# Kernel optimization log

Measured on AMD Instinct MI355X. Metric: run time of the kernel, lower is better.

## Reference

```python
import jax, jax.numpy as jnp
import numpy as np

EPS = 1e-4


def bin_act(x):
    # row-wise standardize (torch std is unbiased, ddof=1) then XNOR-style binarize
    mu = x.mean(axis=1, keepdims=True)
    sd = x.std(axis=1, ddof=1, keepdims=True)
    xn = (x - mu) / (sd + EPS)
    alpha = jnp.abs(xn).mean(axis=1, keepdims=True)  # L1 norm / n
    return alpha * jnp.sign(xn)


def bin_linear(inp, w, b):
    # BinLinearFunction.forward: w_hat = sign(w) * (||w_row||_1 / n_in)
    n = w.shape[1]
    m = jnp.abs(w).sum(axis=1, keepdims=True) / n
    w_hat = jnp.sign(w) * m
    return inp @ w_hat.T + b


def scatter_mean(feat, dst, n_dst):
    s = jax.ops.segment_sum(feat, dst, num_segments=n_dst)
    cnt = jax.ops.segment_sum(jnp.ones(dst.shape, feat.dtype), dst, num_segments=n_dst)
    return s / jnp.maximum(cnt, 1.0)[:, None]


def sage_layer(x, src, dst, n_dst, w_rel, b_rel, w_root, b_root):
    xb = bin_act(x)
    xt = bin_act(x[:n_dst])
    agg = scatter_mean(xb[src], dst, n_dst)  # mean aggregation of binarized neighbors
    return bin_linear(agg, w_rel, b_rel) + bin_linear(xt, w_root, b_root)


def setup_inputs() -> dict:
    key = jax.random.key(0)
    ks = jax.random.split(key, 10)
    N0, N1, N2 = 512000, 20480, 2048
    E1, E2 = 512000, 20480
    IN, HID, OUT = 128, 256, 64
    x = jax.random.normal(ks[0], (N0, IN), dtype=jnp.float32)
    src1 = jax.random.randint(ks[1], (E1,), 0, N0)
    dst1 = jax.random.randint(ks[2], (E1,), 0, N1)
    src2 = jax.random.randint(ks[3], (E2,), 0, N1)
    dst2 = jax.random.randint(ks[4], (E2,), 0, N2)
    def winit(k, out_f, in_f):
        return jax.random.normal(k, (out_f, in_f), dtype=jnp.float32) * np.sqrt(1.0 / in_f)
    return {
        "x": x, "src1": src1, "dst1": dst1, "src2": src2, "dst2": dst2,
        "w_rel1": winit(ks[5], HID, IN), "b_rel1": jnp.zeros((HID,), jnp.float32),
        "w_root1": winit(ks[6], HID, IN), "b_root1": jnp.zeros((HID,), jnp.float32),
        "w_rel2": winit(ks[7], OUT, HID), "b_rel2": jnp.zeros((OUT,), jnp.float32),
        "w_root2": winit(ks[8], OUT, HID), "b_root2": jnp.zeros((OUT,), jnp.float32),
        "n1": N1, "n2": N2,
    }


def reference(x, src1, dst1, src2, dst2, w_rel1, b_rel1, w_root1, b_root1,
              w_rel2, b_rel2, w_root2, b_root2, n1, n2):
    h = sage_layer(x, src1, dst1, n1, w_rel1, b_rel1, w_root1, b_root1)
    h = jax.nn.relu(h)  # dropout p=0.0
    h = sage_layer(h, src2, dst2, n2, w_rel2, b_rel2, w_root2, b_root2)
    return jax.nn.log_softmax(h, axis=-1)
```

## Files before the change

### kernel.cpp

```cpp
#include <hip/hip_runtime.h>
#include <stdint.h>

typedef unsigned long long u64;
typedef float nfloat4 __attribute__((ext_vector_type(4)));


#define CAP1 128
#define CAP2 128

__device__ __forceinline__ void pack_row128(
    float4 v0, float4 v1, float4 v2, float4 v3, float mu, int c,
    u64& w0, u64& w1)
{
  unsigned m = 0;
  m |= (v0.x > mu) ? 1u << 0  : 0u;
  m |= (v0.y > mu) ? 1u << 1  : 0u;
  m |= (v0.z > mu) ? 1u << 2  : 0u;
  m |= (v0.w > mu) ? 1u << 3  : 0u;
  m |= (v1.x > mu) ? 1u << 4  : 0u;
  m |= (v1.y > mu) ? 1u << 5  : 0u;
  m |= (v1.z > mu) ? 1u << 6  : 0u;
  m |= (v1.w > mu) ? 1u << 7  : 0u;
  m |= (v2.x > mu) ? 1u << 8  : 0u;
  m |= (v2.y > mu) ? 1u << 9  : 0u;
  m |= (v2.z > mu) ? 1u << 10 : 0u;
  m |= (v2.w > mu) ? 1u << 11 : 0u;
  m |= (v3.x > mu) ? 1u << 12 : 0u;
  m |= (v3.y > mu) ? 1u << 13 : 0u;
  m |= (v3.z > mu) ? 1u << 14 : 0u;
  m |= (v3.w > mu) ? 1u << 15 : 0u;
  u64 wv = (u64)m << (16 * (c & 3));
  wv |= __shfl_xor(wv, 1);
  wv |= __shfl_xor(wv, 2);
  u64 other = __shfl_xor(wv, 4);
  w0 = (c & 4) ? other : wv;
  w1 = (c & 4) ? wv : other;
}

__device__ __forceinline__ void prep_w128_block(
    const float* __restrict__ w, int rowbase, int tid,
    ulonglong2* __restrict__ wbits, float* __restrict__ m)
{
  int lane = tid & 63;
  int g = lane >> 3, c = lane & 7;
  int row = rowbase + (tid >> 6) * 8 + g;
  const float4* wr = (const float4*)(w + (size_t)row * 128);
  float4 v0 = wr[c];
  float4 v1 = wr[c + 8];
  float4 v2 = wr[c + 16];
  float4 v3 = wr[c + 24];
  float s = fabsf(v0.x) + fabsf(v0.y) + fabsf(v0.z) + fabsf(v0.w)
          + fabsf(v1.x) + fabsf(v1.y) + fabsf(v1.z) + fabsf(v1.w)
          + fabsf(v2.x) + fabsf(v2.y) + fabsf(v2.z) + fabsf(v2.w)
          + fabsf(v3.x) + fabsf(v3.y) + fabsf(v3.z) + fabsf(v3.w);
  s += __shfl_xor(s, 1); s += __shfl_xor(s, 2); s += __shfl_xor(s, 4);
  u64 w0, w1;
  pack_row128(v0, v1, v2, v3, 0.0f, c, w0, w1);
  if (c == 0) {
    wbits[row] = make_ulonglong2(w0, w1);
    m[row] = s * (1.0f / 128.0f);
  }
}

__device__ __forceinline__ void prep_w256_block(
    const float* __restrict__ w, int rowbase, int tid,
    u64* __restrict__ wbits, float* __restrict__ m)
{
  int lane = tid & 63;
  int o = rowbase + (tid >> 6);
  const float* wr = w + (size_t)o * 256;
  float s = 0.0f;
  u64 b[4];
  #pragma unroll
  for (int wd = 0; wd < 4; wd++) {
    float v = wr[wd * 64 + lane];
    s += fabsf(v);
    b[wd] = __ballot(v > 0.0f);
  }
  #pragma unroll
  for (int off = 32; off > 0; off >>= 1) s += __shfl_xor(s, off);
  if (lane == 0) {
    wbits[o * 4 + 0] = b[0]; wbits[o * 4 + 1] = b[1];
    wbits[o * 4 + 2] = b[2]; wbits[o * 4 + 3] = b[3];
    m[o] = s * (1.0f / 256.0f);
  }
}

__global__ __launch_bounds__(256) void prep_all_kernel(
    const float* __restrict__ w_rel1, const float* __restrict__ w_root1,
    const float* __restrict__ w_rel2, const float* __restrict__ w_root2,
    ulonglong2* __restrict__ wbr1, float* __restrict__ m_r1,
    ulonglong2* __restrict__ wbt1, float* __restrict__ m_t1,
    u64* __restrict__ wbr2, float* __restrict__ m_r2,
    u64* __restrict__ wbt2, float* __restrict__ m_t2,
    int* __restrict__ cnt, int cntn,
    int* __restrict__ markw, int markn)
{
  int b = blockIdx.x, t = threadIdx.x;
  if (b < 8) {
    prep_w128_block(w_rel1, b * 32, t, wbr1, m_r1);
  } else if (b < 16) {
    prep_w128_block(w_root1, (b - 8) * 32, t, wbt1, m_t1);
  } else if (b < 32) {
    prep_w256_block(w_rel2, (b - 16) * 4, t, wbr2, m_r2);
  } else if (b < 48) {
    prep_w256_block(w_root2, (b - 32) * 4, t, wbt2, m_t2);
  } else if (b < 59) {
    int base = (b - 48) * 2048 + t * 8;
    #pragma unroll
    for (int k = 0; k < 8; k++) {
      int i = base + k;
      if (i < cntn) cnt[i] = 0;
    }
  } else {
    int base = (b - 59) * 2048 + t * 8;
    #pragma unroll
    for (int k = 0; k < 8; k++) {
      int i = base + k;
      if (i < markn) markw[i] = 0;
    }
  }
}

__global__ void scatter_direct_kernel(
    const int* __restrict__ dst1, const int* __restrict__ src1, int E1,
    int* __restrict__ cnt1, int* __restrict__ slots1,
    const int* __restrict__ dst2, const int* __restrict__ src2, int E2,
    int* __restrict__ cnt2, int* __restrict__ slots2,
    unsigned char* __restrict__ mark)
{
  int i = blockIdx.x * blockDim.x + threadIdx.x;
  if (i < E1) {
    int s = src1[i];
    mark[s] = 1;
    int dd = dst1[i];
    int p = atomicAdd(&cnt1[dd], 1);
    if (p < CAP1) slots1[(size_t)dd * CAP1 + p] = s;
  } else if (i < E1 + E2) {
    int j = i - E1;
    int dd = dst2[j];
    int p = atomicAdd(&cnt2[dd], 1);
    if (p < CAP2) slots2[(size_t)dd * CAP2 + p] = src2[j];
  }
}

__global__ __launch_bounds__(256) void binact128_kernel(
    const float* __restrict__ x, const unsigned char* __restrict__ mark,
    int n1, u64* __restrict__ rec)
{
  int lane = threadIdx.x & 63;
  int wid  = blockIdx.x * 4 + (threadIdx.x >> 6);
  int g = lane >> 3;
  int c = lane & 7;
  int row = wid * 8 + g;
  if (row >= n1 && mark[row] == 0) return;

  const nfloat4* xr = (const nfloat4*)(x + (size_t)row * 128);
  nfloat4 n0 = __builtin_nontemporal_load(xr + c);
  nfloat4 n1v = __builtin_nontemporal_load(xr + c + 8);
  nfloat4 n2 = __builtin_nontemporal_load(xr + c + 16);
  nfloat4 n3 = __builtin_nontemporal_load(xr + c + 24);
  float4 v0 = make_float4(n0.x, n0.y, n0.z, n0.w);
  float4 v1 = make_float4(n1v.x, n1v.y, n1v.z, n1v.w);
  float4 v2 = make_float4(n2.x, n2.y, n2.z, n2.w);
  float4 v3 = make_float4(n3.x, n3.y, n3.z, n3.w);

  float s = (v0.x + v0.y + v0.z + v0.w) + (v1.x + v1.y + v1.z + v1.w)
          + (v2.x + v2.y + v2.z + v2.w) + (v3.x + v3.y + v3.z + v3.w);
  s += __shfl_xor(s, 1); s += __shfl_xor(s, 2); s += __shfl_xor(s, 4);
  float mu = s * (1.0f / 128.0f);

  float ss = 0.f, sa = 0.f;
  {
    float d;
    d = v0.x - mu; ss += d * d; sa += fabsf(d);
    d = v0.y - mu; ss += d * d; sa += fabsf(d);
    d = v0.z - mu; ss += d * d; sa += fabsf(d);
    d = v0.w - mu; ss += d * d; sa += fabsf(d);
    d = v1.x - mu; ss += d * d; sa += fabsf(d);
    d = v1.y - mu; ss += d * d; sa += fabsf(d);
    d = v1.z - mu; ss += d * d; sa += fabsf(d);
    d = v1.w - mu; ss += d * d; sa += fabsf(d);
    d = v2.x - mu; ss += d * d; sa += fabsf(d);
    d = v2.y - mu; ss += d * d; sa += fabsf(d);
    d = v2.z - mu; ss += d * d; sa += fabsf(d);
    d = v2.w - mu; ss += d * d; sa += fabsf(d);
    d = v3.x - mu; ss += d * d; sa += fabsf(d);
    d = v3.y - mu; ss += d * d; sa += fabsf(d);
    d = v3.z - mu; ss += d * d; sa += fabsf(d);
    d = v3.w - mu; ss += d * d; sa += fabsf(d);
  }
  ss += __shfl_xor(ss, 1); ss += __shfl_xor(ss, 2); ss += __shfl_xor(ss, 4);
  sa += __shfl_xor(sa, 1); sa += __shfl_xor(sa, 2); sa += __shfl_xor(sa, 4);
  float sd = sqrtf(ss * (1.0f / 127.0f));
  float a  = __fdividef(sa * (1.0f / 128.0f), sd + 1e-4f);

  u64 w0, w1;
  pack_row128(v0, v1, v2, v3, mu, c, w0, w1);
  if (c == 0) {
    u64* rp = rec + (size_t)row * 4;
    *(ulonglong2*)rp = make_ulonglong2(w0, w1);
    ((float*)rp)[4] = a;
  }
}

__global__ __launch_bounds__(256) void layer1_kernel(
    const u64* __restrict__ rec,
    const int* __restrict__ cnt, const int* __restrict__ slots,
    const ulonglong2* __restrict__ wb_rel, const float* __restrict__ m_rel,
    const float* __restrict__ b_rel,
    const ulonglong2* __restrict__ wb_root, const float* __restrict__ m_root,
    const float* __restrict__ b_root,
    u64* __restrict__ bits2, float* __restrict__ alpha2)
{
  int lane = threadIdx.x & 63;
  int d = blockIdx.x * 4 + (threadIdx.x >> 6);

  ulonglong2 wr[4], wt[4];
  float mr[4], br[4], mt[4], bt[4];
  #pragma unroll
  for (int j = 0; j < 4; j++) {
    int f = j * 64 + lane;
    wr[j] = wb_rel[f];  mr[j] = m_rel[f];  br[j] = b_rel[f];
    wt[j] = wb_root[f]; mt[j] = m_root[f]; bt[j] = b_root[f];
  }

  int deg = cnt[d];
  int degc = min(deg, CAP1);
  const int* slot = slots + (size_t)d * CAP1;

  float acc2[4] = {0.f, 0.f, 0.f, 0.f};
  float suma = 0.f;

  #pragma unroll 4
  for (int e = 0; e < degc; e++) {
    int sn = __builtin_amdgcn_readfirstlane(slot[e]);
    const u64* rp = rec + (size_t)sn * 4;
    ulonglong2 bb = *(const ulonglong2*)rp;
    float a = ((const float*)rp)[4];
    suma += a;
    #pragma unroll
    for (int j = 0; j < 4; j++) {
      int pc = __popcll(bb.x ^ wr[j].x) + __popcll(bb.y ^ wr[j].y);
      acc2[j] += a * (float)pc;
    }
  }

  const u64* rd = rec + (size_t)d * 4;
  ulonglong2 xb = *(const ulonglong2*)rd;
  float ax = ((const float*)rd)[4];

  float invc = (deg > 0) ? 1.0f / (float)deg : 1.0f;
  float z[4];
  #pragma unroll
  for (int j = 0; j < 4; j++) {
    int pcr = __popcll(xb.x ^ wt[j].x) + __popcll(xb.y ^ wt[j].y);
    float rel = mr[j] * (128.0f * suma - 2.0f * acc2[j]) * invc + br[j];
    float rot = mt[j] * ax * (float)(128 - 2 * pcr) + bt[j];
    z[j] = fmaxf(rel + rot, 0.0f);
  }

  float s = z[0] + z[1] + z[2] + z[3];
  #pragma unroll
  for (int off = 1; off < 64; off <<= 1) s += __shfl_xor(s, off);
  float mu = s * (1.0f / 256.0f);
  float ss = 0.f, sa = 0.f;
  #pragma unroll
  for (int j = 0; j < 4; j++) {
    float dv = z[j] - mu;
    ss += dv * dv; sa += fabsf(dv);
  }
  #pragma unroll
  for (int off = 1; off < 64; off <<= 1) {
    ss += __shfl_xor(ss, off);
    sa += __shfl_xor(sa, off);
  }
  float sd = sqrtf(ss * (1.0f / 255.0f));
  float a2 = __fdividef(sa * (1.0f / 256.0f), sd + 1e-4f);
  u64 wd0 = __ballot(z[0] > mu);
  u64 wd1 = __ballot(z[1] > mu);
  u64 wd2 = __ballot(z[2] > mu);
  u64 wd3 = __ballot(z[3] > mu);
  if (lane == 0) {
    ulonglong2* bp = (ulonglong2*)(bits2 + (size_t)d * 4);
    bp[0] = make_ulonglong2(wd0, wd1);
    bp[1] = make_ulonglong2(wd2, wd3);
    alpha2[d] = a2;
  }
}

__global__ __launch_bounds__(256) void layer2_kernel(
    const u64* __restrict__ bits2, const float* __restrict__ alpha2,
    const int* __restrict__ cnt, const int* __restrict__ slots,
    const u64* __restrict__ wb_rel, const float* __restrict__ m_rel,
    const float* __restrict__ b_rel,
    const u64* __restrict__ wb_root, const float* __restrict__ m_root,
    const float* __restrict__ b_root,
    float* __restrict__ out)
{
  int d = blockIdx.x * 4 + (threadIdx.x >> 6);
  int o = threadIdx.x & 63;
  u64 w0 = wb_rel[o * 4 + 0], w1 = wb_rel[o * 4 + 1];
  u64 w2 = wb_rel[o * 4 + 2], w3 = wb_rel[o * 4 + 3];
  int deg = cnt[d];
  int degc = min(deg, CAP2);
  const int* slot = slots + (size_t)d * CAP2;
  float acc = 0.0f;
  #pragma unroll 2
  for (int e = 0; e < degc; e++) {
    int sn = __builtin_amdgcn_readfirstlane(slot[e]);
    const ulonglong2* bp = (const ulonglong2*)(bits2 + (size_t)sn * 4);
    ulonglong2 p0 = bp[0], p1 = bp[1];
    float a = alpha2[sn];
    int pc = __popcll(p0.x ^ w0) + __popcll(p0.y ^ w1)
           + __popcll(p1.x ^ w2) + __popcll(p1.y ^ w3);
    acc += a * (float)(256 - 2 * pc);
  }
  float invc = 1.0f / (float)(deg > 0 ? deg : 1);
  const u64* xp = bits2 + (size_t)d * 4;
  float ax = alpha2[d];
  int pcr = __popcll(xp[0] ^ wb_root[o * 4 + 0]) + __popcll(xp[1] ^ wb_root[o * 4 + 1])
          + __popcll(xp[2] ^ wb_root[o * 4 + 2]) + __popcll(xp[3] ^ wb_root[o * 4 + 3]);
  float z = m_rel[o] * acc * invc + b_rel[o]
          + m_root[o] * ax * (float)(256 - 2 * pcr) + b_root[o];
  float mx = z;
  #pragma unroll
  for (int off = 32; off > 0; off >>= 1) mx = fmaxf(mx, __shfl_xor(mx, off));
  float ex = expf(z - mx);
  float se = ex;
  #pragma unroll
  for (int off = 32; off > 0; off >>= 1) se += __shfl_xor(se, off);
  out[(size_t)d * 64 + o] = z - mx - logf(se);
}

extern "C" void kernel_launch(void* const* d_in, const int* in_sizes, int n_in,
                              void* d_out, int out_size, void* d_ws, size_t ws_size,
                              hipStream_t stream)
{
  const float* x       = (const float*)d_in[0];
  const int*   src1    = (const int*)d_in[1];
  const int*   dst1    = (const int*)d_in[2];
  const int*   src2    = (const int*)d_in[3];
  const int*   dst2    = (const int*)d_in[4];
  const float* w_rel1  = (const float*)d_in[5];
  const float* b_rel1  = (const float*)d_in[6];
  const float* w_root1 = (const float*)d_in[7];
  const float* b_root1 = (const float*)d_in[8];
  const float* w_rel2  = (const float*)d_in[9];
  const float* b_rel2  = (const float*)d_in[10];
  const float* w_root2 = (const float*)d_in[11];
  const float* b_root2 = (const float*)d_in[12];

  const int IN  = 128;
  const int HID = in_sizes[6];
  const int OUT = in_sizes[10];
  const int N0  = in_sizes[0] / IN;
  const int E1  = in_sizes[1];
  const int E2  = in_sizes[3];
  const int N1  = 20480;
  const int N2  = out_size / OUT;
  (void)n_in; (void)ws_size;

  char* p = (char*)d_ws;
  auto alloc = [&](size_t bytes) {
    char* r = p;
    p += (bytes + 255) & ~(size_t)255;
    return r;
  };
  u64*   rec    = (u64*)alloc((size_t)N0 * 32);
  u64*   bits2  = (u64*)alloc((size_t)N1 * 32);
  float* alpha2 = (float*)alloc((size_t)N1 * 4);
  int*   slots1 = (int*)alloc((size_t)N1 * CAP1 * 4);
  int*   slots2 = (int*)alloc((size_t)N2 * CAP2 * 4);
  int*   cnt1   = (int*)alloc((size_t)(N1 + N2) * 4);
  int*   cnt2   = cnt1 + N1;
  unsigned char* mark = (unsigned char*)alloc((size_t)N0);
  ulonglong2* wbr1 = (ulonglong2*)alloc((size_t)HID * 16);
  ulonglong2* wbt1 = (ulonglong2*)alloc((size_t)HID * 16);
  u64*   wbr2   = (u64*)alloc((size_t)OUT * 32);
  u64*   wbt2   = (u64*)alloc((size_t)OUT * 32);
  float* m_r1   = (float*)alloc((size_t)HID * 4);
  float* m_t1   = (float*)alloc((size_t)HID * 4);
  float* m_r2   = (float*)alloc((size_t)OUT * 4);
  float* m_t2   = (float*)alloc((size_t)OUT * 4);

  prep_all_kernel<<<122, 256, 0, stream>>>(
      w_rel1, w_root1, w_rel2, w_root2,
      wbr1, m_r1, wbt1, m_t1, wbr2, m_r2, wbt2, m_t2,
      cnt1, N1 + N2, (int*)mark, N0 / 4);

  scatter_direct_kernel<<<(E1 + E2 + 255) / 256, 256, 0, stream>>>(
      dst1, src1, E1, cnt1, slots1, dst2, src2, E2, cnt2, slots2, mark);

  binact128_kernel<<<N0 / 32, 256, 0, stream>>>(x, mark, N1, rec);

  layer1_kernel<<<N1 / 4, 256, 0, stream>>>(rec, cnt1, slots1,
                                            wbr1, m_r1, b_rel1, wbt1, m_t1, b_root1,
                                            bits2, alpha2);

  layer2_kernel<<<N2 / 4, 256, 0, stream>>>(bits2, alpha2, cnt2, slots2,
                                            wbr2, m_r2, b_rel2, wbt2, m_t2, b_root2,
                                            (float*)d_out);
}
```

Baseline: 458.7 us.

## Fuse all stages into one persistent cooperative kernel with grid syncs

```diff
diff --git a/kernel.cpp b/kernel.cpp
--- a/kernel.cpp
+++ b/kernel.cpp
@@ -1,12 +1,32 @@
 #include <hip/hip_runtime.h>
+#include <hip/hip_cooperative_groups.h>
 #include <stdint.h>
 
+namespace cg = cooperative_groups;
 typedef unsigned long long u64;
 typedef float nfloat4 __attribute__((ext_vector_type(4)));
 
 
 #define CAP1 128
 #define CAP2 128
+#define NBLK 512
+#define NTHR 256
+
+struct Params {
+  const float* x;
+  const int *src1, *dst1, *src2, *dst2;
+  const float *w_rel1, *b_rel1, *w_root1, *b_root1;
+  const float *w_rel2, *b_rel2, *w_root2, *b_root2;
+  u64* rec;
+  u64* bits2; float* alpha2;
+  int *slots1, *slots2, *cnt1, *cnt2;
+  unsigned char* mark;
+  ulonglong2 *wbr1, *wbt1;
+  u64 *wbr2, *wbt2;
+  float *m_r1, *m_t1, *m_r2, *m_t2;
+  float* out;
+  int E1, E2, N0, N1, N2;
+};
 
 __device__ __forceinline__ void pack_row128(
     float4 v0, float4 v1, float4 v2, float4 v3, float mu, int c,
@@ -86,271 +106,275 @@
   }
 }
 
-__global__ __launch_bounds__(256) void prep_all_kernel(
-    const float* __restrict__ w_rel1, const float* __restrict__ w_root1,
-    const float* __restrict__ w_rel2, const float* __restrict__ w_root2,
-    ulonglong2* __restrict__ wbr1, float* __restrict__ m_r1,
-    ulonglong2* __restrict__ wbt1, float* __restrict__ m_t1,
-    u64* __restrict__ wbr2, float* __restrict__ m_r2,
-    u64* __restrict__ wbt2, float* __restrict__ m_t2,
-    int* __restrict__ cnt, int cntn,
-    int* __restrict__ markw, int markn)
-{
-  int b = blockIdx.x, t = threadIdx.x;
-  if (b < 8) {
-    prep_w128_block(w_rel1, b * 32, t, wbr1, m_r1);
-  } else if (b < 16) {
-    prep_w128_block(w_root1, (b - 8) * 32, t, wbt1, m_t1);
-  } else if (b < 32) {
-    prep_w256_block(w_rel2, (b - 16) * 4, t, wbr2, m_r2);
-  } else if (b < 48) {
-    prep_w256_block(w_root2, (b - 32) * 4, t, wbt2, m_t2);
-  } else if (b < 59) {
-    int base = (b - 48) * 2048 + t * 8;
-    #pragma unroll
-    for (int k = 0; k < 8; k++) {
-      int i = base + k;
-      if (i < cntn) cnt[i] = 0;
-    }
-  } else {
-    int base = (b - 59) * 2048 + t * 8;
-    #pragma unroll
-    for (int k = 0; k < 8; k++) {
-      int i = base + k;
-      if (i < markn) markw[i] = 0;
-    }
-  }
-}
-
-__global__ void scatter_direct_kernel(
-    const int* __restrict__ dst1, const int* __restrict__ src1, int E1,
-    int* __restrict__ cnt1, int* __restrict__ slots1,
-    const int* __restrict__ dst2, const int* __restrict__ src2, int E2,
-    int* __restrict__ cnt2, int* __restrict__ slots2,
-    unsigned char* __restrict__ mark)
-{
-  int i = blockIdx.x * blockDim.x + threadIdx.x;
-  if (i < E1) {
-    int s = src1[i];
-    mark[s] = 1;
-    int dd = dst1[i];
-    int p = atomicAdd(&cnt1[dd], 1);
-    if (p < CAP1) slots1[(size_t)dd * CAP1 + p] = s;
-  } else if (i < E1 + E2) {
-    int j = i - E1;
-    int dd = dst2[j];
-    int p = atomicAdd(&cnt2[dd], 1);
-    if (p < CAP2) slots2[(size_t)dd * CAP2 + p] = src2[j];
-  }
-}
-
-__global__ __launch_bounds__(256) void binact128_kernel(
-    const float* __restrict__ x, const unsigned char* __restrict__ mark,
-    int n1, u64* __restrict__ rec)
-{
-  int lane = threadIdx.x & 63;
-  int wid  = blockIdx.x * 4 + (threadIdx.x >> 6);
-  int g = lane >> 3;
-  int c = lane & 7;
-  int row = wid * 8 + g;
-  if (row >= n1 && mark[row] == 0) return;
-
-  const nfloat4* xr = (const nfloat4*)(x + (size_t)row * 128);
-  nfloat4 n0 = __builtin_nontemporal_load(xr + c);
-  nfloat4 n1v = __builtin_nontemporal_load(xr + c + 8);
-  nfloat4 n2 = __builtin_nontemporal_load(xr + c + 16);
-  nfloat4 n3 = __builtin_nontemporal_load(xr + c + 24);
-  float4 v0 = make_float4(n0.x, n0.y, n0.z, n0.w);
-  float4 v1 = make_float4(n1v.x, n1v.y, n1v.z, n1v.w);
-  float4 v2 = make_float4(n2.x, n2.y, n2.z, n2.w);
-  float4 v3 = make_float4(n3.x, n3.y, n3.z, n3.w);
-
-  float s = (v0.x + v0.y + v0.z + v0.w) + (v1.x + v1.y + v1.z + v1.w)
-          + (v2.x + v2.y + v2.z + v2.w) + (v3.x + v3.y + v3.z + v3.w);
-  s += __shfl_xor(s, 1); s += __shfl_xor(s, 2); s += __shfl_xor(s, 4);
-  float mu = s * (1.0f / 128.0f);
-
-  float ss = 0.f, sa = 0.f;
-  {
-    float d;
-    d = v0.x - mu; ss += d * d; sa += fabsf(d);
-    d = v0.y - mu; ss += d * d; sa += fabsf(d);
-    d = v0.z - mu; ss += d * d; sa += fabsf(d);
-    d = v0.w - mu; ss += d * d; sa += fabsf(d);
-    d = v1.x - mu; ss += d * d; sa += fabsf(d);
-    d = v1.y - mu; ss += d * d; sa += fabsf(d);
-    d = v1.z - mu; ss += d * d; sa += fabsf(d);
-    d = v1.w - mu; ss += d * d; sa += fabsf(d);
-    d = v2.x - mu; ss += d * d; sa += fabsf(d);
-    d = v2.y - mu; ss += d * d; sa += fabsf(d);
-    d = v2.z - mu; ss += d * d; sa += fabsf(d);
-    d = v2.w - mu; ss += d * d; sa += fabsf(d);
-    d = v3.x - mu; ss += d * d; sa += fabsf(d);
-    d = v3.y - mu; ss += d * d; sa += fabsf(d);
-    d = v3.z - mu; ss += d * d; sa += fabsf(d);
-    d = v3.w - mu; ss += d * d; sa += fabsf(d);
-  }
-  ss += __shfl_xor(ss, 1); ss += __shfl_xor(ss, 2); ss += __shfl_xor(ss, 4);
-  sa += __shfl_xor(sa, 1); sa += __shfl_xor(sa, 2); sa += __shfl_xor(sa, 4);
-  float sd = sqrtf(ss * (1.0f / 127.0f));
-  float a  = __fdividef(sa * (1.0f / 128.0f), sd + 1e-4f);
-
-  u64 w0, w1;
-  pack_row128(v0, v1, v2, v3, mu, c, w0, w1);
-  if (c == 0) {
-    u64* rp = rec + (size_t)row * 4;
-    *(ulonglong2*)rp = make_ulonglong2(w0, w1);
-    ((float*)rp)[4] = a;
-  }
-}
-
-__global__ __launch_bounds__(256) void layer1_kernel(
-    const u64* __restrict__ rec,
-    const int* __restrict__ cnt, const int* __restrict__ slots,
-    const ulonglong2* __restrict__ wb_rel, const float* __restrict__ m_rel,
-    const float* __restrict__ b_rel,
-    const ulonglong2* __restrict__ wb_root, const float* __restrict__ m_root,
-    const float* __restrict__ b_root,
-    u64* __restrict__ bits2, float* __restrict__ alpha2)
-{
-  int lane = threadIdx.x & 63;
-  int d = blockIdx.x * 4 + (threadIdx.x >> 6);
-
+
+__device__ __forceinline__ void phase_wprep(const Params& P, int bid, int tid)
+{
+  if (bid < 8) {
+    prep_w128_block(P.w_rel1, bid * 32, tid, P.wbr1, P.m_r1);
+  } else if (bid < 16) {
+    prep_w128_block(P.w_root1, (bid - 8) * 32, tid, P.wbt1, P.m_t1);
+  } else if (bid < 32) {
+    prep_w256_block(P.w_rel2, (bid - 16) * 4, tid, P.wbr2, P.m_r2);
+  } else if (bid < 48) {
+    prep_w256_block(P.w_root2, (bid - 32) * 4, tid, P.wbt2, P.m_t2);
+  }
+}
+
+__device__ __forceinline__ void phase_zero(const Params& P, int gthread, int nthreads)
+{
+  int cntn = P.N1 + P.N2;
+  for (int i = gthread; i < cntn; i += nthreads) P.cnt1[i] = 0;
+  int* markw = (int*)P.mark;
+  int markn = P.N0 >> 2;
+  for (int i = gthread; i < markn; i += nthreads) markw[i] = 0;
+}
+
+__device__ __forceinline__ void phase_scatter(const Params& P, int gthread, int nthreads)
+{
+  int tot = P.E1 + P.E2;
+  for (int i = gthread; i < tot; i += nthreads) {
+    if (i < P.E1) {
+      int s = P.src1[i];
+      P.mark[s] = 1;
+      int dd = P.dst1[i];
+      int p = atomicAdd(&P.cnt1[dd], 1);
+      if (p < CAP1) P.slots1[(size_t)dd * CAP1 + p] = s;
+    } else {
+      int j = i - P.E1;
+      int dd = P.dst2[j];
+      int p = atomicAdd(&P.cnt2[dd], 1);
+      if (p < CAP2) P.slots2[(size_t)dd * CAP2 + p] = P.src2[j];
+    }
+  }
+}
+
+__device__ __forceinline__ void phase_binact(const Params& P, int waveId, int nWaves, int lane)
+{
+  int njobs = P.N0 >> 3;
+  int g = lane >> 3, c = lane & 7;
+  for (int j = waveId; j < njobs; j += nWaves) {
+    int row = j * 8 + g;
+    if (row < P.N1 || P.mark[row] != 0) {
+      const nfloat4* xr = (const nfloat4*)(P.x + (size_t)row * 128);
+      nfloat4 n0 = __builtin_nontemporal_load(xr + c);
+      nfloat4 n1v = __builtin_nontemporal_load(xr + c + 8);
+      nfloat4 n2 = __builtin_nontemporal_load(xr + c + 16);
+      nfloat4 n3 = __builtin_nontemporal_load(xr + c + 24);
+      float4 v0 = make_float4(n0.x, n0.y, n0.z, n0.w);
+      float4 v1 = make_float4(n1v.x, n1v.y, n1v.z, n1v.w);
+      float4 v2 = make_float4(n2.x, n2.y, n2.z, n2.w);
+      float4 v3 = make_float4(n3.x, n3.y, n3.z, n3.w);
+
+      float s = (v0.x + v0.y + v0.z + v0.w) + (v1.x + v1.y + v1.z + v1.w)
+              + (v2.x + v2.y + v2.z + v2.w) + (v3.x + v3.y + v3.z + v3.w);
+      s += __shfl_xor(s, 1); s += __shfl_xor(s, 2); s += __shfl_xor(s, 4);
+      float mu = s * (1.0f / 128.0f);
+
+      float ss = 0.f, sa = 0.f;
+      {
+        float d;
+        d = v0.x - mu; ss += d * d; sa += fabsf(d);
+        d = v0.y - mu; ss += d * d; sa += fabsf(d);
+        d = v0.z - mu; ss += d * d; sa += fabsf(d);
+        d = v0.w - mu; ss += d * d; sa += fabsf(d);
+        d = v1.x - mu; ss += d * d; sa += fabsf(d);
+        d = v1.y - mu; ss += d * d; sa += fabsf(d);
+        d = v1.z - mu; ss += d * d; sa += fabsf(d);
+        d = v1.w - mu; ss += d * d; sa += fabsf(d);
+        d = v2.x - mu; ss += d * d; sa += fabsf(d);
+        d = v2.y - mu; ss += d * d; sa += fabsf(d);
+        d = v2.z - mu; ss += d * d; sa += fabsf(d);
+        d = v2.w - mu; ss += d * d; sa += fabsf(d);
+        d = v3.x - mu; ss += d * d; sa += fabsf(d);
+        d = v3.y - mu; ss += d * d; sa += fabsf(d);
+        d = v3.z - mu; ss += d * d; sa += fabsf(d);
+        d = v3.w - mu; ss += d * d; sa += fabsf(d);
+      }
+      ss += __shfl_xor(ss, 1); ss += __shfl_xor(ss, 2); ss += __shfl_xor(ss, 4);
+      sa += __shfl_xor(sa, 1); sa += __shfl_xor(sa, 2); sa += __shfl_xor(sa, 4);
+      float sd = sqrtf(ss * (1.0f / 127.0f));
+      float a  = __fdividef(sa * (1.0f / 128.0f), sd + 1e-4f);
+
+      u64 w0, w1;
+      pack_row128(v0, v1, v2, v3, mu, c, w0, w1);
+      if (c == 0) {
+        u64* rp = P.rec + (size_t)row * 4;
+        *(ulonglong2*)rp = make_ulonglong2(w0, w1);
+        ((float*)rp)[4] = a;
+      }
+    }
+  }
+}
+
+__device__ __forceinline__ void phase_layer1(const Params& P, int waveId, int nWaves, int lane)
+{
   ulonglong2 wr[4], wt[4];
   float mr[4], br[4], mt[4], bt[4];
   #pragma unroll
   for (int j = 0; j < 4; j++) {
     int f = j * 64 + lane;
-    wr[j] = wb_rel[f];  mr[j] = m_rel[f];  br[j] = b_rel[f];
-    wt[j] = wb_root[f]; mt[j] = m_root[f]; bt[j] = b_root[f];
-  }
-
-  int deg = cnt[d];
-  int degc = min(deg, CAP1);
-  const int* slot = slots + (size_t)d * CAP1;
-
-  float acc2[4] = {0.f, 0.f, 0.f, 0.f};
-  float suma = 0.f;
-
-  #pragma unroll 4
-  for (int e = 0; e < degc; e++) {
-    int sn = __builtin_amdgcn_readfirstlane(slot[e]);
-    const u64* rp = rec + (size_t)sn * 4;
-    ulonglong2 bb = *(const ulonglong2*)rp;
-    float a = ((const float*)rp)[4];
-    suma += a;
+    wr[j] = P.wbr1[f]; mr[j] = P.m_r1[f]; br[j] = P.b_rel1[f];
+    wt[j] = P.wbt1[f]; mt[j] = P.m_t1[f]; bt[j] = P.b_root1[f];
+  }
+  for (int d = waveId; d < P.N1; d += nWaves) {
+    int deg = P.cnt1[d];
+    int degc = min(deg, CAP1);
+    const int* slot = P.slots1 + (size_t)d * CAP1;
+
+    float acc2[4] = {0.f, 0.f, 0.f, 0.f};
+    float suma = 0.f;
+    #pragma unroll 4
+    for (int e = 0; e < degc; e++) {
+      int sn = __builtin_amdgcn_readfirstlane(slot[e]);
+      const u64* rp = P.rec + (size_t)sn * 4;
+      ulonglong2 bb = *(const ulonglong2*)rp;
+      float a = ((const float*)rp)[4];
+      suma += a;
+      #pragma unroll
+      for (int j = 0; j < 4; j++) {
+        int pc = __popcll(bb.x ^ wr[j].x) + __popcll(bb.y ^ wr[j].y);
+        acc2[j] += a * (float)pc;
+      }
+    }
+
+    const u64* rd = P.rec + (size_t)d * 4;
+    ulonglong2 xb = *(const ulonglong2*)rd;
+    float ax = ((const float*)rd)[4];
+
+    float invc = (deg > 0) ? 1.0f / (float)deg : 1.0f;
+    float z[4];
     #pragma unroll
     for (int j = 0; j < 4; j++) {
-      int pc = __popcll(bb.x ^ wr[j].x) + __popcll(bb.y ^ wr[j].y);
-      acc2[j] += a * (float)pc;
-    }
-  }
-
-  const u64* rd = rec + (size_t)d * 4;
-  ulonglong2 xb = *(const ulonglong2*)rd;
-  float ax = ((const float*)rd)[4];
-
-  float invc = (deg > 0) ? 1.0f / (float)deg : 1.0f;
-  float z[4];
-  #pragma unroll
-  for (int j = 0; j < 4; j++) {
-    int pcr = __popcll(xb.x ^ wt[j].x) + __popcll(xb.y ^ wt[j].y);
-    float rel = mr[j] * (128.0f * suma - 2.0f * acc2[j]) * invc + br[j];
-    float rot = mt[j] * ax * (float)(128 - 2 * pcr) + bt[j];
-    z[j] = fmaxf(rel + rot, 0.0f);
-  }
-
-  float s = z[0] + z[1] + z[2] + z[3];
-  #pragma unroll
-  for (int off = 1; off < 64; off <<= 1) s += __shfl_xor(s, off);
-  float mu = s * (1.0f / 256.0f);
-  float ss = 0.f, sa = 0.f;
-  #pragma unroll
-  for (int j = 0; j < 4; j++) {
-    float dv = z[j] - mu;
-    ss += dv * dv; sa += fabsf(dv);
-  }
-  #pragma unroll
-  for (int off = 1; off < 64; off <<= 1) {
-    ss += __shfl_xor(ss, off);
-    sa += __shfl_xor(sa, off);
-  }
-  float sd = sqrtf(ss * (1.0f / 255.0f));
-  float a2 = __fdividef(sa * (1.0f / 256.0f), sd + 1e-4f);
-  u64 wd0 = __ballot(z[0] > mu);
-  u64 wd1 = __ballot(z[1] > mu);
-  u64 wd2 = __ballot(z[2] > mu);
-  u64 wd3 = __ballot(z[3] > mu);
-  if (lane == 0) {
-    ulonglong2* bp = (ulonglong2*)(bits2 + (size_t)d * 4);
-    bp[0] = make_ulonglong2(wd0, wd1);
-    bp[1] = make_ulonglong2(wd2, wd3);
-    alpha2[d] = a2;
-  }
-}
-
-__global__ __launch_bounds__(256) void layer2_kernel(
-    const u64* __restrict__ bits2, const float* __restrict__ alpha2,
-    const int* __restrict__ cnt, const int* __restrict__ slots,
-    const u64* __restrict__ wb_rel, const float* __restrict__ m_rel,
-    const float* __restrict__ b_rel,
-    const u64* __restrict__ wb_root, const float* __restrict__ m_root,
-    const float* __restrict__ b_root,
-    float* __restrict__ out)
-{
-  int d = blockIdx.x * 4 + (threadIdx.x >> 6);
-  int o = threadIdx.x & 63;
-  u64 w0 = wb_rel[o * 4 + 0], w1 = wb_rel[o * 4 + 1];
-  u64 w2 = wb_rel[o * 4 + 2], w3 = wb_rel[o * 4 + 3];
-  int deg = cnt[d];
-  int degc = min(deg, CAP2);
-  const int* slot = slots + (size_t)d * CAP2;
-  float acc = 0.0f;
-  #pragma unroll 2
-  for (int e = 0; e < degc; e++) {
-    int sn = __builtin_amdgcn_readfirstlane(slot[e]);
-    const ulonglong2* bp = (const ulonglong2*)(bits2 + (size_t)sn * 4);
-    ulonglong2 p0 = bp[0], p1 = bp[1];
-    float a = alpha2[sn];
-    int pc = __popcll(p0.x ^ w0) + __popcll(p0.y ^ w1)
-           + __popcll(p1.x ^ w2) + __popcll(p1.y ^ w3);
-    acc += a * (float)(256 - 2 * pc);
-  }
-  float invc = 1.0f / (float)(deg > 0 ? deg : 1);
-  const u64* xp = bits2 + (size_t)d * 4;
-  float ax = alpha2[d];
-  int pcr = __popcll(xp[0] ^ wb_root[o * 4 + 0]) + __popcll(xp[1] ^ wb_root[o * 4 + 1])
-          + __popcll(xp[2] ^ wb_root[o * 4 + 2]) + __popcll(xp[3] ^ wb_root[o * 4 + 3]);
-  float z = m_rel[o] * acc * invc + b_rel[o]
-          + m_root[o] * ax * (float)(256 - 2 * pcr) + b_root[o];
-  float mx = z;
-  #pragma unroll
-  for (int off = 32; off > 0; off >>= 1) mx = fmaxf(mx, __shfl_xor(mx, off));
-  float ex = expf(z - mx);
-  float se = ex;
-  #pragma unroll
-  for (int off = 32; off > 0; off >>= 1) se += __shfl_xor(se, off);
-  out[(size_t)d * 64 + o] = z - mx - logf(se);
+      int pcr = __popcll(xb.x ^ wt[j].x) + __popcll(xb.y ^ wt[j].y);
+      float rel = mr[j] * (128.0f * suma - 2.0f * acc2[j]) * invc + br[j];
+      float rot = mt[j] * ax * (float)(128 - 2 * pcr) + bt[j];
+      z[j] = fmaxf(rel + rot, 0.0f);
+    }
+
+    float s = z[0] + z[1] + z[2] + z[3];
+    #pragma unroll
+    for (int off = 1; off < 64; off <<= 1) s += __shfl_xor(s, off);
+    float mu = s * (1.0f / 256.0f);
+    float ss = 0.f, sa = 0.f;
+    #pragma unroll
+    for (int j = 0; j < 4; j++) {
+      float dv = z[j] - mu;
+      ss += dv * dv; sa += fabsf(dv);
+    }
+    #pragma unroll
+    for (int off = 1; off < 64; off <<= 1) {
+      ss += __shfl_xor(ss, off);
+      sa += __shfl_xor(sa, off);
+    }
+    float sd = sqrtf(ss * (1.0f / 255.0f));
+    float a2 = __fdividef(sa * (1.0f / 256.0f), sd + 1e-4f);
+    u64 wd0 = __ballot(z[0] > mu);
+    u64 wd1 = __ballot(z[1] > mu);
+    u64 wd2 = __ballot(z[2] > mu);
+    u64 wd3 = __ballot(z[3] > mu);
+    if (lane == 0) {
+      ulonglong2* bp = (ulonglong2*)(P.bits2 + (size_t)d * 4);
+      bp[0] = make_ulonglong2(wd0, wd1);
+      bp[1] = make_ulonglong2(wd2, wd3);
+      P.alpha2[d] = a2;
+    }
+  }
+}
+
+__device__ __forceinline__ void phase_layer2(const Params& P, int waveId, int nWaves, int lane)
+{
+  int o = lane;
+  u64 w0 = P.wbr2[o * 4 + 0], w1 = P.wbr2[o * 4 + 1];
+  u64 w2 = P.wbr2[o * 4 + 2], w3 = P.wbr2[o * 4 + 3];
+  u64 t0 = P.wbt2[o * 4 + 0], t1 = P.wbt2[o * 4 + 1];
+  u64 t2 = P.wbt2[o * 4 + 2], t3 = P.wbt2[o * 4 + 3];
+  float mrel = P.m_r2[o], brel = P.b_rel2[o];
+  float mrot = P.m_t2[o], brot = P.b_root2[o];
+  for (int d = waveId; d < P.N2; d += nWaves) {
+    int deg = P.cnt2[d];
+    int degc = min(deg, CAP2);
+    const int* slot = P.slots2 + (size_t)d * CAP2;
+    float acc = 0.0f;
+    #pragma unroll 2
+    for (int e = 0; e < degc; e++) {
+      int sn = __builtin_amdgcn_readfirstlane(slot[e]);
+      const ulonglong2* bp = (const ulonglong2*)(P.bits2 + (size_t)sn * 4);
+      ulonglong2 p0 = bp[0], p1 = bp[1];
+      float a = P.alpha2[sn];
+      int pc = __popcll(p0.x ^ w0) + __popcll(p0.y ^ w1)
+             + __popcll(p1.x ^ w2) + __popcll(p1.y ^ w3);
+      acc += a * (float)(256 - 2 * pc);
+    }
+    float invc = 1.0f / (float)(deg > 0 ? deg : 1);
+    const u64* xp = P.bits2 + (size_t)d * 4;
+    float ax = P.alpha2[d];
+    int pcr = __popcll(xp[0] ^ t0) + __popcll(xp[1] ^ t1)
+            + __popcll(xp[2] ^ t2) + __popcll(xp[3] ^ t3);
+    float z = mrel * acc * invc + brel
+            + mrot * ax * (float)(256 - 2 * pcr) + brot;
+    float mx = z;
+    #pragma unroll
+    for (int off = 32; off > 0; off >>= 1) mx = fmaxf(mx, __shfl_xor(mx, off));
+    float ex = expf(z - mx);
+    float se = ex;
+    #pragma unroll
+    for (int off = 32; off > 0; off >>= 1) se += __shfl_xor(se, off);
+    P.out[(size_t)d * 64 + o] = z - mx - logf(se);
+  }
+}
+
+__global__ __launch_bounds__(NTHR, 2) void fused_kernel(Params P)
+{
+  cg::grid_group grid = cg::this_grid();
+  const int tid = threadIdx.x;
+  const int bid = blockIdx.x;
+  const int gthread = bid * NTHR + tid;
+  const int nthreads = NBLK * NTHR;
+  const int lane = tid & 63;
+  const int waveId = gthread >> 6;
+  const int nWaves = nthreads >> 6;
+
+  phase_wprep(P, bid, tid);
+  phase_zero(P, gthread, nthreads);
+  __threadfence(); grid.sync(); __threadfence();
+  phase_scatter(P, gthread, nthreads);
+  __threadfence(); grid.sync(); __threadfence();
+  phase_binact(P, waveId, nWaves, lane);
+  __threadfence(); grid.sync(); __threadfence();
+  phase_layer1(P, waveId, nWaves, lane);
+  __threadfence(); grid.sync(); __threadfence();
+  phase_layer2(P, waveId, nWaves, lane);
+}
+
+__global__ __launch_bounds__(NTHR) void k_prep(Params P)
+{
+  phase_wprep(P, blockIdx.x, threadIdx.x);
+  phase_zero(P, blockIdx.x * NTHR + threadIdx.x, gridDim.x * NTHR);
+}
+__global__ __launch_bounds__(NTHR) void k_scatter(Params P)
+{
+  phase_scatter(P, blockIdx.x * NTHR + threadIdx.x, gridDim.x * NTHR);
+}
+__global__ __launch_bounds__(NTHR) void k_binact(Params P)
+{
+  int g = blockIdx.x * NTHR + threadIdx.x;
+  phase_binact(P, g >> 6, (gridDim.x * NTHR) >> 6, threadIdx.x & 63);
+}
+__global__ __launch_bounds__(NTHR) void k_layer1(Params P)
+{
+  int g = blockIdx.x * NTHR + threadIdx.x;
+  phase_layer1(P, g >> 6, (gridDim.x * NTHR) >> 6, threadIdx.x & 63);
+}
+__global__ __launch_bounds__(NTHR) void k_layer2(Params P)
+{
+  int g = blockIdx.x * NTHR + threadIdx.x;
+  phase_layer2(P, g >> 6, (gridDim.x * NTHR) >> 6, threadIdx.x & 63);
 }
 
 extern "C" void kernel_launch(void* const* d_in, const int* in_sizes, int n_in,
                               void* d_out, int out_size, void* d_ws, size_t ws_size,
                               hipStream_t stream)
 {
-  const float* x       = (const float*)d_in[0];
-  const int*   src1    = (const int*)d_in[1];
-  const int*   dst1    = (const int*)d_in[2];
-  const int*   src2    = (const int*)d_in[3];
-  const int*   dst2    = (const int*)d_in[4];
-  const float* w_rel1  = (const float*)d_in[5];
-  const float* b_rel1  = (const float*)d_in[6];
-  const float* w_root1 = (const float*)d_in[7];
-  const float* b_root1 = (const float*)d_in[8];
-  const float* w_rel2  = (const float*)d_in[9];
-  const float* b_rel2  = (const float*)d_in[10];
-  const float* w_root2 = (const float*)d_in[11];
-  const float* b_root2 = (const float*)d_in[12];
-
   const int IN  = 128;
   const int HID = in_sizes[6];
   const int OUT = in_sizes[10];
@@ -384,21 +408,37 @@
   float* m_r2   = (float*)alloc((size_t)OUT * 4);
   float* m_t2   = (float*)alloc((size_t)OUT * 4);
 
-  prep_all_kernel<<<122, 256, 0, stream>>>(
-      w_rel1, w_root1, w_rel2, w_root2,
-      wbr1, m_r1, wbt1, m_t1, wbr2, m_r2, wbt2, m_t2,
-      cnt1, N1 + N2, (int*)mark, N0 / 4);
-
-  scatter_direct_kernel<<<(E1 + E2 + 255) / 256, 256, 0, stream>>>(
-      dst1, src1, E1, cnt1, slots1, dst2, src2, E2, cnt2, slots2, mark);
-
-  binact128_kernel<<<N0 / 32, 256, 0, stream>>>(x, mark, N1, rec);
-
-  layer1_kernel<<<N1 / 4, 256, 0, stream>>>(rec, cnt1, slots1,
-                                            wbr1, m_r1, b_rel1, wbt1, m_t1, b_root1,
-                                            bits2, alpha2);
-
-  layer2_kernel<<<N2 / 4, 256, 0, stream>>>(bits2, alpha2, cnt2, slots2,
-                                            wbr2, m_r2, b_rel2, wbt2, m_t2, b_root2,
-                                            (float*)d_out);
-}
+  Params P;
+  P.x = (const float*)d_in[0];
+  P.src1 = (const int*)d_in[1];
+  P.dst1 = (const int*)d_in[2];
+  P.src2 = (const int*)d_in[3];
+  P.dst2 = (const int*)d_in[4];
+  P.w_rel1 = (const float*)d_in[5];
+  P.b_rel1 = (const float*)d_in[6];
+  P.w_root1 = (const float*)d_in[7];
+  P.b_root1 = (const float*)d_in[8];
+  P.w_rel2 = (const float*)d_in[9];
+  P.b_rel2 = (const float*)d_in[10];
+  P.w_root2 = (const float*)d_in[11];
+  P.b_root2 = (const float*)d_in[12];
+  P.rec = rec; P.bits2 = bits2; P.alpha2 = alpha2;
+  P.slots1 = slots1; P.slots2 = slots2; P.cnt1 = cnt1; P.cnt2 = cnt2;
+  P.mark = mark;
+  P.wbr1 = wbr1; P.wbt1 = wbt1; P.wbr2 = wbr2; P.wbt2 = wbt2;
+  P.m_r1 = m_r1; P.m_t1 = m_t1; P.m_r2 = m_r2; P.m_t2 = m_t2;
+  P.out = (float*)d_out;
+  P.E1 = E1; P.E2 = E2; P.N0 = N0; P.N1 = N1; P.N2 = N2;
+
+  void* args[] = { &P };
+  hipError_t err = hipLaunchCooperativeKernel((const void*)fused_kernel,
+                                              dim3(NBLK), dim3(NTHR), args,
+                                              0, stream);
+  if (err != hipSuccess) {
+    k_prep   <<<128,                     NTHR, 0, stream>>>(P);
+    k_scatter<<<(E1 + E2 + NTHR - 1) / NTHR, NTHR, 0, stream>>>(P);
+    k_binact <<<N0 / 32,                 NTHR, 0, stream>>>(P);
+    k_layer1 <<<N1 / 4,                  NTHR, 0, stream>>>(P);
+    k_layer2 <<<N2 / 4,                  NTHR, 0, stream>>>(P);
+  }
+}
```

Result: slower. 1.163 ms (+153.6%).
